# Optimization experiments

Measured on AMD Instinct MI355X. Metric: run time of the kernel, lower is better.

## Reference

```python
import jax, jax.numpy as jnp
import numpy as np

N_NODES, N_EDGES = 100000, 1600000
D_IN, D_H, D_OUT = 256, 128, 32


def _gcn_conv(x, W, b, row, col, norm, n):
    # GCNConv: transform, normalized gather from source nodes, scatter-sum at targets, bias.
    h = x @ W                                   # [n, d_out]
    msgs = h[row] * norm[:, None]               # [E', d_out] edge messages
    out = jax.ops.segment_sum(msgs, col, num_segments=n)
    return out + b


def setup_inputs() -> dict:
    key = jax.random.key(0)
    k = jax.random.split(key, 6)
    x = jax.random.normal(k[0], (N_NODES, D_IN), dtype=jnp.float32)
    edge_index = jax.random.randint(k[1], (2, N_EDGES), 0, N_NODES, dtype=jnp.int64)
    # Glorot-ish scaled params (GCNConv lin has no bias; bias added post-aggregation)
    W1 = jax.random.normal(k[2], (D_IN, D_H), dtype=jnp.float32) * (1.0 / np.sqrt(D_IN))
    b1 = jnp.zeros((D_H,), dtype=jnp.float32)
    W2 = jax.random.normal(k[3], (D_H, D_OUT), dtype=jnp.float32) * (1.0 / np.sqrt(D_H))
    b2 = jnp.zeros((D_OUT,), dtype=jnp.float32)
    return {"x": x, "W1": W1, "b1": b1, "W2": W2, "b2": b2, "edge_index": edge_index}


def reference(x, W1, b1, W2, b2, edge_index):
    n = x.shape[0]
    loops = jnp.arange(n, dtype=edge_index.dtype)
    row = jnp.concatenate([edge_index[0], loops])   # sources (incl. self-loops)
    col = jnp.concatenate([edge_index[1], loops])   # targets
    # symmetric normalization deg^{-1/2} (deg >= 1 because of self-loops)
    deg = jax.ops.segment_sum(jnp.ones_like(col, dtype=x.dtype), col, num_segments=n)
    dinv = deg ** -0.5
    norm = dinv[row] * dinv[col]
    h = jax.nn.relu(_gcn_conv(x, W1, b1, row, col, norm, n))
    # F.dropout(training=False) is identity in eval mode
    out = _gcn_conv(h, W2, b2, row, col, norm, n)
    return jax.nn.log_softmax(out, axis=1)
```

## Files before the change

kernel.cpp:

```cpp
#include <hip/hip_runtime.h>
#include <math.h>

#define N_NODES 100000
#define N_EDGES 1600000
#define D_IN 256
#define D_H 128
#define D_OUT 32
#define N_PAD 102400
#define NB 196
#define CAPB 10240
#define CHUNK 4096

typedef long long ll;
typedef unsigned int uint;
typedef unsigned short ushort;
typedef unsigned char uchar;
typedef short frag_ab __attribute__((ext_vector_type(8)));
typedef float frag_cd __attribute__((ext_vector_type(4)));

__device__ __forceinline__ ushort f2bf(float f) {
    uint u = __float_as_uint(f);
    u += 0x7FFFu + ((u >> 16) & 1u);
    return (ushort)(u >> 16);
}
__device__ __forceinline__ float bfl(uint u) { return __uint_as_float(u << 16); }
__device__ __forceinline__ float bfh(uint u) { return __uint_as_float(u & 0xFFFF0000u); }
__device__ __forceinline__ uint packbf(float a, float b) {
    return (uint)f2bf(a) | ((uint)f2bf(b) << 16);
}

__global__ __launch_bounds__(256) void k_prep(const float* __restrict__ W1,
                                              const float* __restrict__ W2,
                                              ushort* __restrict__ w1t,
                                              ushort* __restrict__ w2t,
                                              int* __restrict__ gcur) {
    int gi = blockIdx.x * 256 + threadIdx.x;
    if (blockIdx.x == 0) gcur[threadIdx.x] = 0;
    if (gi < D_IN * D_H) {
        int k = gi >> 7, nn = gi & 127;
        w1t[nn * D_IN + k] = f2bf(W1[gi]);
    } else if (gi < D_IN * D_H + D_H * D_OUT) {
        int j = gi - D_IN * D_H;
        int k = j >> 5, nn = j & 31;
        w2t[nn * D_H + k] = f2bf(W2[j]);
    }
}

__global__ __launch_bounds__(256, 3) void k_fused(const int* __restrict__ row,
                                                  const int* __restrict__ col,
                                                  int* __restrict__ gcur,
                                                  uint* __restrict__ pairs,
                                                  const float* __restrict__ x,
                                                  const ushort* __restrict__ w1t,
                                                  ushort* __restrict__ hxs,
                                                  int n, int e) {
    __shared__ int cnt[NB];
    __shared__ int lofs[NB];
    __shared__ int lstart[NB];
    __shared__ int sc[256];
    __shared__ uint spair[CHUNK];
    __shared__ uchar sbuck[CHUNK];
    const int t = threadIdx.x;
    const int GA = (e + CHUNK - 1) / CHUNK;
    const int bid = blockIdx.x;

    if (bid < GA) {
        const int id = bid;
        for (int i = t; i < NB; i += 256) cnt[i] = 0;
        __syncthreads();
        const int base = id * CHUNK;
        const int end = min(base + CHUNK, e);
        const int valid = end - base;
        int rs[16], cs[16];
#pragma unroll
        for (int j = 0; j < 16; j++) {
            int idx = base + t + j * 256;
            bool ok = idx < end;
            int c = ok ? col[idx] : 0;
            rs[j] = ok ? row[idx] : 0;
            cs[j] = ok ? c : -1;
            if (ok) atomicAdd(&cnt[c >> 9], 1);
        }
        __syncthreads();
        int v = (t < NB) ? cnt[t] : 0;
        sc[t] = v;
        __syncthreads();
        for (int o = 1; o < 256; o <<= 1) {
            int u2 = (t >= o) ? sc[t - o] : 0;
            __syncthreads();
            sc[t] += u2;
            __syncthreads();
        }
        if (t < NB) {
            lofs[t] = sc[t] - v;
            lstart[t] = (v > 0) ? atomicAdd(&gcur[t], v) : 0;
            cnt[t] = 0;
        }
        __syncthreads();
#pragma unroll
        for (int j = 0; j < 16; j++) {
            int c = cs[j];
            if (c >= 0) {
                int b = c >> 9;
                int pos = lofs[b] + atomicAdd(&cnt[b], 1);
                spair[pos] = ((uint)rs[j] << 9) | (uint)(c & 511);
                sbuck[pos] = (uchar)b;
            }
        }
        __syncthreads();
        for (int i = t; i < valid; i += 256) {
            int b = sbuck[i];
            int rel = lstart[b] + (i - lofs[b]);
            if (rel < CAPB) pairs[b * CAPB + rel] = spair[i];
        }
    } else {
        const int id = bid - GA;
        const int wv = t >> 6, lane = t & 63;
        const int lm = lane & 15, quad = lane >> 4;
        const int base = id * 128 + wv * 32;

        frag_cd acc[2][8];
#pragma unroll
        for (int mt = 0; mt < 2; mt++)
#pragma unroll
            for (int nt = 0; nt < 8; nt++) acc[mt][nt] = (frag_cd){0.f, 0.f, 0.f, 0.f};

        const float4* xr[2];
#pragma unroll
        for (int mt = 0; mt < 2; mt++) {
            int node = base + mt * 16 + lm;
            xr[mt] = (const float4*)(x + (ll)min(node, n - 1) * D_IN);
        }

#pragma unroll
        for (int ks = 0; ks < 8; ks++) {
            frag_ab a[2];
#pragma unroll
            for (int mt = 0; mt < 2; mt++) {
                float4 v0 = xr[mt][ks * 8 + quad * 2];
                float4 v1 = xr[mt][ks * 8 + quad * 2 + 1];
                uint* ap = (uint*)&a[mt];
                ap[0] = packbf(v0.x, v0.y);
                ap[1] = packbf(v0.z, v0.w);
                ap[2] = packbf(v1.x, v1.y);
                ap[3] = packbf(v1.z, v1.w);
            }
#pragma unroll
            for (int nt = 0; nt < 8; nt++) {
                frag_ab b = *(const frag_ab*)&w1t[(nt * 16 + lm) * D_IN + ks * 32 + quad * 8];
#pragma unroll
                for (int mt = 0; mt < 2; mt++)
                    acc[mt][nt] = __builtin_amdgcn_mfma_f32_16x16x32_bf16(
                        a[mt], b, acc[mt][nt], 0, 0, 0);
            }
        }

#pragma unroll
        for (int mt = 0; mt < 2; mt++) {
#pragma unroll
            for (int r = 0; r < 4; r++) {
                int node = base + mt * 16 + quad * 4 + r;
                if (node < n) {
#pragma unroll
                    for (int nt = 0; nt < 8; nt++)
                        hxs[(ll)node * D_H + nt * 16 + lm] = f2bf(acc[mt][nt][r]);
                }
            }
        }
    }
}

__global__ __launch_bounds__(512) void k_fillB(const uint* __restrict__ pairs,
                                               const int* __restrict__ gcur,
                                               int* __restrict__ deg,
                                               int* __restrict__ rp,
                                               float* __restrict__ dinv,
                                               int* __restrict__ csr_src, int n) {
    __shared__ int scsr[CAPB];
    __shared__ int hcnt[512];
    __shared__ int cur[512];
    __shared__ int ssum[512];
    const int b = blockIdx.x, t = threadIdx.x;
    const int node0 = b << 9;
    hcnt[t] = 0;
    __syncthreads();
    const int cnt = min(gcur[b], CAPB);
    const uint* pr = pairs + b * CAPB;
    for (int i = t; i < cnt; i += 512) atomicAdd(&hcnt[pr[i] & 511], 1);
    __syncthreads();
    int d = hcnt[t];
    ssum[t] = d;
    __syncthreads();
    for (int o = 1; o < 512; o <<= 1) {
        int u2 = (t >= o) ? ssum[t - o] : 0;
        __syncthreads();
        ssum[t] += u2;
        __syncthreads();
    }
    int excl = ssum[t] - d;
    cur[t] = excl;
    {
        int vv = node0 + t;
        if (vv < n) {
            rp[vv] = b * CAPB + excl;
            deg[vv] = d;
            dinv[vv] = rsqrtf((float)(1 + d));
        }
    }
    __syncthreads();
    for (int i = t; i < cnt; i += 512) {
        uint pp = pr[i];
        int pos = atomicAdd(&cur[pp & 511], 1);
        if (pos < CAPB) scsr[pos] = (int)(pp >> 9);
    }
    __syncthreads();
    for (int i = t; i < cnt; i += 512)
        csr_src[b * CAPB + i] = scsr[i];
}

__global__ __launch_bounds__(256) void k_agg1(const uint* __restrict__ hxs,
                                              const int* __restrict__ csr_src,
                                              const int* __restrict__ rp,
                                              const int* __restrict__ deg,
                                              const float* __restrict__ dinv,
                                              const float* __restrict__ b1,
                                              uint* __restrict__ h, int n) {
    int v = blockIdx.x * 4 + (threadIdx.x >> 6);
    if (v >= n) return;
    int lane = threadIdx.x & 63;
    float dv = dinv[v];
    uint u = hxs[v * 64 + lane];
    float a0 = dv * bfl(u), a1 = dv * bfh(u);
    int s = rp[v], e = s + deg[v];
    int i = s;
    for (; i + 7 < e; i += 8) {
        int s0 = csr_src[i], s1 = csr_src[i + 1];
        int s2 = csr_src[i + 2], s3 = csr_src[i + 3];
        int s4 = csr_src[i + 4], s5 = csr_src[i + 5];
        int s6 = csr_src[i + 6], s7 = csr_src[i + 7];
        float n0 = dinv[s0], n1 = dinv[s1], n2 = dinv[s2], n3 = dinv[s3];
        float n4 = dinv[s4], n5 = dinv[s5], n6 = dinv[s6], n7 = dinv[s7];
        uint u0 = hxs[s0 * 64 + lane], u1 = hxs[s1 * 64 + lane];
        uint u2 = hxs[s2 * 64 + lane], u3 = hxs[s3 * 64 + lane];
        uint u4 = hxs[s4 * 64 + lane], u5 = hxs[s5 * 64 + lane];
        uint u6 = hxs[s6 * 64 + lane], u7 = hxs[s7 * 64 + lane];
        a0 = fmaf(n0, bfl(u0), a0); a0 = fmaf(n1, bfl(u1), a0);
        a0 = fmaf(n2, bfl(u2), a0); a0 = fmaf(n3, bfl(u3), a0);
        a0 = fmaf(n4, bfl(u4), a0); a0 = fmaf(n5, bfl(u5), a0);
        a0 = fmaf(n6, bfl(u6), a0); a0 = fmaf(n7, bfl(u7), a0);
        a1 = fmaf(n0, bfh(u0), a1); a1 = fmaf(n1, bfh(u1), a1);
        a1 = fmaf(n2, bfh(u2), a1); a1 = fmaf(n3, bfh(u3), a1);
        a1 = fmaf(n4, bfh(u4), a1); a1 = fmaf(n5, bfh(u5), a1);
        a1 = fmaf(n6, bfh(u6), a1); a1 = fmaf(n7, bfh(u7), a1);
    }
    for (; i + 1 < e; i += 2) {
        int s0 = csr_src[i], s1 = csr_src[i + 1];
        float n0 = dinv[s0], n1 = dinv[s1];
        uint u0 = hxs[s0 * 64 + lane], u1 = hxs[s1 * 64 + lane];
        a0 = fmaf(n0, bfl(u0), a0); a0 = fmaf(n1, bfl(u1), a0);
        a1 = fmaf(n0, bfh(u0), a1); a1 = fmaf(n1, bfh(u1), a1);
    }
    if (i < e) {
        int s0 = csr_src[i];
        float n0 = dinv[s0];
        uint u0 = hxs[s0 * 64 + lane];
        a0 = fmaf(n0, bfl(u0), a0);
        a1 = fmaf(n0, bfh(u0), a1);
    }
    float2 bb = ((const float2*)b1)[lane];
    h[v * 64 + lane] = packbf(fmaxf(fmaf(dv, a0, bb.x), 0.f),
                              fmaxf(fmaf(dv, a1, bb.y), 0.f));
}

__global__ __launch_bounds__(256) void k_gemm2(const ushort* __restrict__ h,
                                               const ushort* __restrict__ w2t,
                                               const float* __restrict__ dinv,
                                               ushort* __restrict__ hx2s, int n) {
    const int tid = threadIdx.x;
    const int wv = tid >> 6, lane = tid & 63;
    const int lm = lane & 15, quad = lane >> 4;
    const int base = blockIdx.x * 128 + wv * 32;

    frag_cd acc[2][2];
#pragma unroll
    for (int mt = 0; mt < 2; mt++)
#pragma unroll
        for (int nt = 0; nt < 2; nt++) acc[mt][nt] = (frag_cd){0.f, 0.f, 0.f, 0.f};

    const ushort* hr[2];
#pragma unroll
    for (int mt = 0; mt < 2; mt++) {
        int node = base + mt * 16 + lm;
        hr[mt] = h + (ll)min(node, n - 1) * D_H;
    }

#pragma unroll
    for (int ks = 0; ks < 4; ks++) {
        frag_ab a[2], b[2];
#pragma unroll
        for (int mt = 0; mt < 2; mt++)
            a[mt] = *(const frag_ab*)&hr[mt][ks * 32 + quad * 8];
#pragma unroll
        for (int nt = 0; nt < 2; nt++)
            b[nt] = *(const frag_ab*)&w2t[(nt * 16 + lm) * D_H + ks * 32 + quad * 8];
#pragma unroll
        for (int mt = 0; mt < 2; mt++)
#pragma unroll
            for (int nt = 0; nt < 2; nt++)
                acc[mt][nt] = __builtin_amdgcn_mfma_f32_16x16x32_bf16(
                    a[mt], b[nt], acc[mt][nt], 0, 0, 0);
    }

#pragma unroll
    for (int mt = 0; mt < 2; mt++) {
#pragma unroll
        for (int r = 0; r < 4; r++) {
            int node = base + mt * 16 + quad * 4 + r;
            if (node < n) {
                float dv = dinv[node];
#pragma unroll
                for (int nt = 0; nt < 2; nt++)
                    hx2s[(ll)node * D_OUT + nt * 16 + lm] = f2bf(acc[mt][nt][r] * dv);
            }
        }
    }
}

__global__ __launch_bounds__(256) void k_agg2(const uint* __restrict__ hx2s,
                                              const int* __restrict__ csr_src,
                                              const int* __restrict__ rp,
                                              const int* __restrict__ deg,
                                              const float* __restrict__ dinv,
                                              const float* __restrict__ b2,
                                              float2* __restrict__ out, int n) {
    int v = blockIdx.x * 16 + (threadIdx.x >> 4);
    if (v >= n) return;
    int l16 = threadIdx.x & 15;
    uint u = hx2s[v * 16 + l16];
    float a0 = bfl(u), a1 = bfh(u);
    int s = rp[v], e = s + deg[v];
    int i = s;
    for (; i + 7 < e; i += 8) {
        int s0 = csr_src[i], s1 = csr_src[i + 1];
        int s2 = csr_src[i + 2], s3 = csr_src[i + 3];
        int s4 = csr_src[i + 4], s5 = csr_src[i + 5];
        int s6 = csr_src[i + 6], s7 = csr_src[i + 7];
        uint u0 = hx2s[s0 * 16 + l16], u1 = hx2s[s1 * 16 + l16];
        uint u2 = hx2s[s2 * 16 + l16], u3 = hx2s[s3 * 16 + l16];
        uint u4 = hx2s[s4 * 16 + l16], u5 = hx2s[s5 * 16 + l16];
        uint u6 = hx2s[s6 * 16 + l16], u7 = hx2s[s7 * 16 + l16];
        a0 += bfl(u0) + bfl(u1) + bfl(u2) + bfl(u3) + bfl(u4) + bfl(u5) + bfl(u6) + bfl(u7);
        a1 += bfh(u0) + bfh(u1) + bfh(u2) + bfh(u3) + bfh(u4) + bfh(u5) + bfh(u6) + bfh(u7);
    }
    for (; i + 1 < e; i += 2) {
        int s0 = csr_src[i], s1 = csr_src[i + 1];
        uint u0 = hx2s[s0 * 16 + l16], u1 = hx2s[s1 * 16 + l16];
        a0 += bfl(u0) + bfl(u1);
        a1 += bfh(u0) + bfh(u1);
    }
    if (i < e) {
        uint u0 = hx2s[csr_src[i] * 16 + l16];
        a0 += bfl(u0);
        a1 += bfh(u0);
    }
    float dv = dinv[v];
    float2 bb = ((const float2*)b2)[l16];
    float t0 = fmaf(dv, a0, bb.x), t1 = fmaf(dv, a1, bb.y);
    float mx = fmaxf(t0, t1);
#pragma unroll
    for (int m = 8; m >= 1; m >>= 1) mx = fmaxf(mx, __shfl_xor(mx, m));
    float sum = __expf(t0 - mx) + __expf(t1 - mx);
#pragma unroll
    for (int m = 8; m >= 1; m >>= 1) sum += __shfl_xor(sum, m);
    float lse = mx + __logf(sum);
    out[v * 16 + l16] = make_float2(t0 - lse, t1 - lse);
}

extern "C" void kernel_launch(void* const* d_in, const int* in_sizes, int n_in,
                              void* d_out, int out_size, void* d_ws, size_t ws_size,
                              hipStream_t stream) {
    const float* x  = (const float*)d_in[0];
    const float* W1 = (const float*)d_in[1];
    const float* b1 = (const float*)d_in[2];
    const float* W2 = (const float*)d_in[3];
    const float* b2 = (const float*)d_in[4];
    const int*   ei = (const int*)d_in[5];
    const int* row = ei;
    const int* col = ei + N_EDGES;

    int*    ws_i    = (int*)d_ws;
    int*    deg     = ws_i;
    int*    gcur    = ws_i + N_PAD;
    int*    rp      = ws_i + N_PAD + 256;
    float*  dinv    = (float*)(ws_i + 2 * N_PAD + 256);
    int*    csr_src = ws_i + 3 * N_PAD + 256;
    uint*   pairs   = (uint*)(csr_src + NB * CAPB);
    ushort* w1t     = (ushort*)(pairs + NB * CAPB);
    ushort* w2t     = w1t + D_IN * D_H;
    ushort* hxs     = w2t + D_H * D_OUT;
    ushort* h       = hxs + (ll)N_NODES * D_H;
    ushort* hx2s    = h + (ll)N_NODES * D_H;

    const int n = N_NODES, e = N_EDGES;

    k_prep<<<(D_IN * D_H + D_H * D_OUT + 255) / 256, 256, 0, stream>>>(W1, W2, w1t, w2t, gcur);

    const int GA = (e + CHUNK - 1) / CHUNK;
    const int GG = (n + 127) / 128;
    k_fused<<<GA + GG, 256, 0, stream>>>(row, col, gcur, pairs, x, w1t, hxs, n, e);

    k_fillB<<<NB, 512, 0, stream>>>(pairs, gcur, deg, rp, dinv, csr_src, n);
    k_agg1<<<(n + 3) / 4, 256, 0, stream>>>((const uint*)hxs, csr_src, rp, deg, dinv, b1,
                                            (uint*)h, n);
    k_gemm2<<<(n + 127) / 128, 256, 0, stream>>>(h, w2t, dinv, hx2s, n);
    k_agg2<<<(n + 15) / 16, 256, 0, stream>>>((const uint*)hx2s, csr_src, rp, deg, dinv, b2,
                                              (float2*)d_out, n);
}
```

Baseline: 333.3 us.

## Fuse layer-1 aggregation with layer-2 GEMM via LDS staging

After: 328.9 us. About the same (-1.3%).

```diff
diff --git a/kernel.cpp b/kernel.cpp
--- a/kernel.cpp
+++ b/kernel.cpp
@@ -65,10 +65,9 @@
     const int bid = blockIdx.x;
 
     if (bid < GA) {
-        const int id = bid;
-        for (int i = t; i < NB; i += 256) cnt[i] = 0;
-        __syncthreads();
-        const int base = id * CHUNK;
+        if (t < NB) cnt[t] = 0;
+        __syncthreads();
+        const int base = bid * CHUNK;
         const int end = min(base + CHUNK, e);
         const int valid = end - base;
         int rs[16], cs[16];
@@ -218,110 +217,81 @@
         csr_src[b * CAPB + i] = scsr[i];
 }
 
-__global__ __launch_bounds__(256) void k_agg1(const uint* __restrict__ hxs,
-                                              const int* __restrict__ csr_src,
-                                              const int* __restrict__ rp,
-                                              const int* __restrict__ deg,
-                                              const float* __restrict__ dinv,
-                                              const float* __restrict__ b1,
-                                              uint* __restrict__ h, int n) {
-    int v = blockIdx.x * 4 + (threadIdx.x >> 6);
-    if (v >= n) return;
-    int lane = threadIdx.x & 63;
-    float dv = dinv[v];
-    uint u = hxs[v * 64 + lane];
-    float a0 = dv * bfl(u), a1 = dv * bfh(u);
-    int s = rp[v], e = s + deg[v];
-    int i = s;
-    for (; i + 7 < e; i += 8) {
-        int s0 = csr_src[i], s1 = csr_src[i + 1];
-        int s2 = csr_src[i + 2], s3 = csr_src[i + 3];
-        int s4 = csr_src[i + 4], s5 = csr_src[i + 5];
-        int s6 = csr_src[i + 6], s7 = csr_src[i + 7];
-        float n0 = dinv[s0], n1 = dinv[s1], n2 = dinv[s2], n3 = dinv[s3];
-        float n4 = dinv[s4], n5 = dinv[s5], n6 = dinv[s6], n7 = dinv[s7];
-        uint u0 = hxs[s0 * 64 + lane], u1 = hxs[s1 * 64 + lane];
-        uint u2 = hxs[s2 * 64 + lane], u3 = hxs[s3 * 64 + lane];
-        uint u4 = hxs[s4 * 64 + lane], u5 = hxs[s5 * 64 + lane];
-        uint u6 = hxs[s6 * 64 + lane], u7 = hxs[s7 * 64 + lane];
-        a0 = fmaf(n0, bfl(u0), a0); a0 = fmaf(n1, bfl(u1), a0);
-        a0 = fmaf(n2, bfl(u2), a0); a0 = fmaf(n3, bfl(u3), a0);
-        a0 = fmaf(n4, bfl(u4), a0); a0 = fmaf(n5, bfl(u5), a0);
-        a0 = fmaf(n6, bfl(u6), a0); a0 = fmaf(n7, bfl(u7), a0);
-        a1 = fmaf(n0, bfh(u0), a1); a1 = fmaf(n1, bfh(u1), a1);
-        a1 = fmaf(n2, bfh(u2), a1); a1 = fmaf(n3, bfh(u3), a1);
-        a1 = fmaf(n4, bfh(u4), a1); a1 = fmaf(n5, bfh(u5), a1);
-        a1 = fmaf(n6, bfh(u6), a1); a1 = fmaf(n7, bfh(u7), a1);
-    }
-    for (; i + 1 < e; i += 2) {
-        int s0 = csr_src[i], s1 = csr_src[i + 1];
-        float n0 = dinv[s0], n1 = dinv[s1];
-        uint u0 = hxs[s0 * 64 + lane], u1 = hxs[s1 * 64 + lane];
-        a0 = fmaf(n0, bfl(u0), a0); a0 = fmaf(n1, bfl(u1), a0);
-        a1 = fmaf(n0, bfh(u0), a1); a1 = fmaf(n1, bfh(u1), a1);
-    }
-    if (i < e) {
-        int s0 = csr_src[i];
-        float n0 = dinv[s0];
-        uint u0 = hxs[s0 * 64 + lane];
-        a0 = fmaf(n0, bfl(u0), a0);
-        a1 = fmaf(n0, bfh(u0), a1);
-    }
+__global__ __launch_bounds__(256) void k_agg1f(const uint* __restrict__ hxs,
+                                               const int* __restrict__ csr_src,
+                                               const int* __restrict__ rp,
+                                               const int* __restrict__ deg,
+                                               const float* __restrict__ dinv,
+                                               const float* __restrict__ b1,
+                                               const ushort* __restrict__ w2t,
+                                               ushort* __restrict__ hx2s, int n) {
+    __shared__ uint lds_h[16 * 68];
+    const int t = threadIdx.x;
+    const int w = t >> 6, lane = t & 63;
+    const int lm = lane & 15, quad = lane >> 4;
+    const int nbase = blockIdx.x * 16;
+
     float2 bb = ((const float2*)b1)[lane];
-    h[v * 64 + lane] = packbf(fmaxf(fmaf(dv, a0, bb.x), 0.f),
-                              fmaxf(fmaf(dv, a1, bb.y), 0.f));
-}
-
-__global__ __launch_bounds__(256) void k_gemm2(const ushort* __restrict__ h,
-                                               const ushort* __restrict__ w2t,
-                                               const float* __restrict__ dinv,
-                                               ushort* __restrict__ hx2s, int n) {
-    const int tid = threadIdx.x;
-    const int wv = tid >> 6, lane = tid & 63;
-    const int lm = lane & 15, quad = lane >> 4;
-    const int base = blockIdx.x * 128 + wv * 32;
-
-    frag_cd acc[2][2];
-#pragma unroll
-    for (int mt = 0; mt < 2; mt++)
-#pragma unroll
-        for (int nt = 0; nt < 2; nt++) acc[mt][nt] = (frag_cd){0.f, 0.f, 0.f, 0.f};
-
-    const ushort* hr[2];
-#pragma unroll
-    for (int mt = 0; mt < 2; mt++) {
-        int node = base + mt * 16 + lm;
-        hr[mt] = h + (ll)min(node, n - 1) * D_H;
-    }
-
-#pragma unroll
-    for (int ks = 0; ks < 4; ks++) {
-        frag_ab a[2], b[2];
-#pragma unroll
-        for (int mt = 0; mt < 2; mt++)
-            a[mt] = *(const frag_ab*)&hr[mt][ks * 32 + quad * 8];
-#pragma unroll
-        for (int nt = 0; nt < 2; nt++)
-            b[nt] = *(const frag_ab*)&w2t[(nt * 16 + lm) * D_H + ks * 32 + quad * 8];
-#pragma unroll
-        for (int mt = 0; mt < 2; mt++)
-#pragma unroll
-            for (int nt = 0; nt < 2; nt++)
-                acc[mt][nt] = __builtin_amdgcn_mfma_f32_16x16x32_bf16(
-                    a[mt], b[nt], acc[mt][nt], 0, 0, 0);
-    }
-
-#pragma unroll
-    for (int mt = 0; mt < 2; mt++) {
+#pragma unroll
+    for (int q = 0; q < 4; q++) {
+        int v = nbase + w * 4 + q;
+        float dv = dinv[v];
+        uint u = hxs[v * 64 + lane];
+        float a0 = dv * bfl(u), a1 = dv * bfh(u);
+        int s = rp[v], e = s + deg[v];
+        int i = s;
+        for (; i + 7 < e; i += 8) {
+            int s0 = csr_src[i], s1 = csr_src[i + 1];
+            int s2 = csr_src[i + 2], s3 = csr_src[i + 3];
+            int s4 = csr_src[i + 4], s5 = csr_src[i + 5];
+            int s6 = csr_src[i + 6], s7 = csr_src[i + 7];
+            float n0 = dinv[s0], n1 = dinv[s1], n2 = dinv[s2], n3 = dinv[s3];
+            float n4 = dinv[s4], n5 = dinv[s5], n6 = dinv[s6], n7 = dinv[s7];
+            uint u0 = hxs[s0 * 64 + lane], u1 = hxs[s1 * 64 + lane];
+            uint u2 = hxs[s2 * 64 + lane], u3 = hxs[s3 * 64 + lane];
+            uint u4 = hxs[s4 * 64 + lane], u5 = hxs[s5 * 64 + lane];
+            uint u6 = hxs[s6 * 64 + lane], u7 = hxs[s7 * 64 + lane];
+            a0 = fmaf(n0, bfl(u0), a0); a0 = fmaf(n1, bfl(u1), a0);
+            a0 = fmaf(n2, bfl(u2), a0); a0 = fmaf(n3, bfl(u3), a0);
+            a0 = fmaf(n4, bfl(u4), a0); a0 = fmaf(n5, bfl(u5), a0);
+            a0 = fmaf(n6, bfl(u6), a0); a0 = fmaf(n7, bfl(u7), a0);
+            a1 = fmaf(n0, bfh(u0), a1); a1 = fmaf(n1, bfh(u1), a1);
+            a1 = fmaf(n2, bfh(u2), a1); a1 = fmaf(n3, bfh(u3), a1);
+            a1 = fmaf(n4, bfh(u4), a1); a1 = fmaf(n5, bfh(u5), a1);
+            a1 = fmaf(n6, bfh(u6), a1); a1 = fmaf(n7, bfh(u7), a1);
+        }
+        for (; i + 1 < e; i += 2) {
+            int s0 = csr_src[i], s1 = csr_src[i + 1];
+            float n0 = dinv[s0], n1 = dinv[s1];
+            uint u0 = hxs[s0 * 64 + lane], u1 = hxs[s1 * 64 + lane];
+            a0 = fmaf(n0, bfl(u0), a0); a0 = fmaf(n1, bfl(u1), a0);
+            a1 = fmaf(n0, bfh(u0), a1); a1 = fmaf(n1, bfh(u1), a1);
+        }
+        if (i < e) {
+            int s0 = csr_src[i];
+            float n0 = dinv[s0];
+            uint u0 = hxs[s0 * 64 + lane];
+            a0 = fmaf(n0, bfl(u0), a0);
+            a1 = fmaf(n0, bfh(u0), a1);
+        }
+        lds_h[(w * 4 + q) * 68 + lane] = packbf(fmaxf(fmaf(dv, a0, bb.x), 0.f),
+                                                fmaxf(fmaf(dv, a1, bb.y), 0.f));
+    }
+    __syncthreads();
+
+    if (w < 2) {
+        frag_cd acc = (frag_cd){0.f, 0.f, 0.f, 0.f};
+#pragma unroll
+        for (int c = 0; c < 4; c++) {
+            frag_ab a = *(const frag_ab*)&lds_h[lm * 68 + 16 * c + 4 * quad];
+            frag_ab b = *(const frag_ab*)&w2t[(w * 16 + lm) * D_H + c * 32 + quad * 8];
+            acc = __builtin_amdgcn_mfma_f32_16x16x32_bf16(a, b, acc, 0, 0, 0);
+        }
 #pragma unroll
         for (int r = 0; r < 4; r++) {
-            int node = base + mt * 16 + quad * 4 + r;
-            if (node < n) {
-                float dv = dinv[node];
-#pragma unroll
-                for (int nt = 0; nt < 2; nt++)
-                    hx2s[(ll)node * D_OUT + nt * 16 + lm] = f2bf(acc[mt][nt][r] * dv);
-            }
+            int node = nbase + quad * 4 + r;
+            float dv = dinv[node];
+            hx2s[node * D_OUT + w * 16 + lm] = f2bf(acc[r] * dv);
         }
     }
 }
@@ -398,8 +368,8 @@
     ushort* w1t     = (ushort*)(pairs + NB * CAPB);
     ushort* w2t     = w1t + D_IN * D_H;
     ushort* hxs     = w2t + D_H * D_OUT;
-    ushort* h       = hxs + (ll)N_NODES * D_H;
-    ushort* hx2s    = h + (ll)N_NODES * D_H;
+    ushort* h_unused= hxs + (ll)N_NODES * D_H;
+    ushort* hx2s    = h_unused + (ll)N_NODES * D_H;
 
     const int n = N_NODES, e = N_EDGES;
 
@@ -410,9 +380,8 @@
     k_fused<<<GA + GG, 256, 0, stream>>>(row, col, gcur, pairs, x, w1t, hxs, n, e);
 
     k_fillB<<<NB, 512, 0, stream>>>(pairs, gcur, deg, rp, dinv, csr_src, n);
-    k_agg1<<<(n + 3) / 4, 256, 0, stream>>>((const uint*)hxs, csr_src, rp, deg, dinv, b1,
-                                            (uint*)h, n);
-    k_gemm2<<<(n + 127) / 128, 256, 0, stream>>>(h, w2t, dinv, hx2s, n);
+    k_agg1f<<<n / 16, 256, 0, stream>>>((const uint*)hxs, csr_src, rp, deg, dinv, b1,
+                                        w2t, hx2s, n);
     k_agg2<<<(n + 15) / 16, 256, 0, stream>>>((const uint*)hx2s, csr_src, rp, deg, dinv, b2,
                                               (float2*)d_out, n);
 }
```
